# Kernel tuning notes

Hardware: AMD Instinct MI355X
Metric: run time of the kernel (lower is better)

The kernel has to match this reference:

```python
import jax, jax.numpy as jnp
import numpy as np

VOCAB = 128
N_LAYERS = 4
HEAD_DIM = 128
N_HEADS = 16
PAD = 127
HIDDEN = N_HEADS * HEAD_DIM
B, S = 1, 2048
SCALE = 1.0 / float(np.sqrt(HEAD_DIM))


def _intervals(boundary):
    # torch: interval = cumsum(boundary)+1; shifted = roll(1); shifted[:,0]=interval[:,0]
    idx = jnp.cumsum(boundary.astype(jnp.int32), axis=-1) + 1
    sh = jnp.roll(idx, 1, axis=-1)
    return sh.at[:, 0].set(idx[:, 0])


def _build_mask(tokens, segment_mask, specials_mask):
    # Combined causal & padding & word & segment mask, cache_size=0, distances=0.
    word_int = _intervals(specials_mask)            # [B,S]
    seg_bound = ~segment_mask                       # [B,S]
    seg_int = _intervals(seg_bound)                 # [B,S]
    q = jnp.arange(S)[:, None]
    kv = jnp.arange(S)[None, :]
    causal = q >= kv                                # [S,S]
    dist_neg = (q - kv) < 0                         # mask_*_distance = 0 term
    nonpad = tokens != PAD                          # [B,S]
    padm = nonpad[:, :, None] & nonpad[:, None, :]  # [B,S,S]
    wordm = specials_mask[:, None, :] | dist_neg[None] | (word_int[:, :, None] == word_int[:, None, :])
    segm = seg_bound[:, None, :] | dist_neg[None] | (seg_int[:, :, None] == seg_int[:, None, :])
    return causal[None] & padm & wordm & segm       # [B,S,S]


def _attention(h, mask):
    # q=k=v=h (no projections in DummyModel); flex_attention default scale 1/sqrt(D)
    x = h.reshape(B, S, N_HEADS, HEAD_DIM)
    scores = jnp.einsum('bqhd,bkhd->bhqk', x, x) * SCALE
    neg = jnp.finfo(scores.dtype).min
    scores = jnp.where(mask[:, None], scores, neg)
    probs = jax.nn.softmax(scores, axis=-1)
    # fully-masked rows (e.g. padding queries) -> zero output, matching flex_attention
    row_valid = jnp.any(mask, axis=-1)              # [B,S]
    probs = jnp.where(row_valid[:, None, :, None], probs, 0.0)
    out = jnp.einsum('bhqk,bkhd->bqhd', probs, x)
    return out.reshape(B, S, HIDDEN)


def setup_inputs() -> dict:
    key = jax.random.key(0)
    k1, k2, k3, k4, k5, k6 = jax.random.split(key, 6)
    tokens = jax.random.randint(k1, (B, S), 0, PAD)          # 0..126, no pad tokens
    segment_mask = jax.random.bernoulli(k2, 0.98, (B, S))
    specials_mask = jax.random.bernoulli(k3, 0.2, (B, S))    # True = word boundary/special
    emb_w = jax.random.normal(k4, (VOCAB, HIDDEN), jnp.float32) * 0.02
    lm_w = jax.random.normal(k5, (VOCAB, HIDDEN), jnp.float32) * 0.02
    lm_b = jnp.zeros((VOCAB,), jnp.float32)
    seg_w = jax.random.normal(k6, (2, HIDDEN), jnp.float32) * 0.02
    seg_b = jnp.zeros((2,), jnp.float32)
    return {"tokens": tokens, "segment_mask": segment_mask, "specials_mask": specials_mask,
            "emb_w": emb_w, "lm_w": lm_w, "lm_b": lm_b, "seg_w": seg_w, "seg_b": seg_b}


def reference(tokens, segment_mask, specials_mask, emb_w, lm_w, lm_b, seg_w, seg_b):
    mask = _build_mask(tokens, segment_mask, specials_mask)
    hidden = emb_w[tokens]                                   # [B,S,HIDDEN]
    for _ in range(N_LAYERS):
        hidden = _attention(hidden, mask)
    logits = hidden @ lm_w.T + lm_b                          # [B,S,VOCAB]
    logits_segment = hidden @ seg_w.T + seg_b                # [B,S,2]
    return logits, logits_segment
```

## Files before the change

kernel.cpp:

```cpp
#include <hip/hip_runtime.h>

#define S 2048
#define HID 2048
#define NH 16
#define DH 128
#define VOC 128
#define LCAP 128
#define K2EXP 0.12752551286084112f
#define RTHR 62.0f
#define NEGS -3.0e38f

typedef __bf16 bf16_t;
typedef __attribute__((ext_vector_type(8))) __bf16 bf16x8;
typedef __attribute__((ext_vector_type(4))) __bf16 bf16x4;
typedef __attribute__((ext_vector_type(4))) float f32x4;
typedef __attribute__((ext_vector_type(16))) float f32x16;

typedef __attribute__((address_space(1))) unsigned int guint;
typedef __attribute__((address_space(3))) unsigned int luint;

#define MFMA16 __builtin_amdgcn_mfma_f32_16x16x32_bf16
#define MFMA32 __builtin_amdgcn_mfma_f32_32x32x16_bf16

__device__ __forceinline__ void gl_lds16(const void* g, void* l) {
  __builtin_amdgcn_global_load_lds((guint*)(unsigned long long)g,
                                   (luint*)(unsigned)(unsigned long long)l,
                                   16, 0, 0);
}

__device__ __forceinline__ unsigned cvtpk(float lo, float hi) {
  unsigned r;
  asm("v_cvt_pk_bf16_f32 %0, %1, %2" : "=v"(r) : "v"(lo), "v"(hi));
  return r;
}
__device__ __forceinline__ void plswap(unsigned& a, unsigned& b) {
  asm volatile("v_permlane32_swap_b32 %0, %1" : "+v"(a), "+v"(b));
}
__device__ __forceinline__ bf16x8 mk8(unsigned d0, unsigned d1, unsigned d2, unsigned d3) {
  union { unsigned u[4]; bf16x8 v; } x;
  x.u[0] = d0; x.u[1] = d1; x.u[2] = d2; x.u[3] = d3;
  return x.v;
}


__global__ __launch_bounds__(256) void maskprep2(const int* __restrict__ tokens,
                                                 const unsigned char* __restrict__ seg,
                                                 const unsigned char* __restrict__ spc,
                                                 int4* __restrict__ mi,
                                                 int* __restrict__ lq,
                                                 unsigned long long* __restrict__ lmask,
                                                 int2* __restrict__ smeta) {
  __shared__ int ssp[257], ssg[257], smw[257], sms[257], sfl[257];
  __shared__ int fpre[2048];
  __shared__ int ns64[64];
  __shared__ unsigned long long lmk[32];
  __shared__ int cdet[2];
  int t = threadIdx.x;
  if (t < 2) cdet[t] = 0;
  if (t < 32) lmk[t] = 0ull;
  __syncthreads();
  {
    int nz = ((t & 3) != 0 && seg[t]) ? 1 : 0;
    int fc = ((t & 3) == 3 && seg[t] == 0x3f) ? 1 : 0;
    if (nz) atomicAdd(&cdet[0], 1);
    if (fc) atomicAdd(&cdet[1], 1);
  }
  __syncthreads();
  int lay = (cdet[1] > 8) ? 2 : ((cdet[0] > 4) ? 1 : 0);
  auto getb = [&](const unsigned char* p, int i) -> int {
    if (lay == 1) return p[i] != 0;
    if (lay == 2) return ((const float*)p)[i] != 0.f;
    return ((const int*)p)[i] != 0;
  };
  int base = t * 8;
  int spv[8], sgv[8], npv[8], fv[8];
  int a = 0, b = 0, mw = 0, ms = 0, fs = 0;
  for (int j = 0; j < 8; j++) {
    int i = base + j;
    spv[j] = getb(spc, i);
    sgv[j] = 1 - getb(seg, i);
    npv[j] = (tokens[i] != 127) ? 1 : 0;
    fv[j] = spv[j] & sgv[j] & npv[j];
    a += spv[j]; b += sgv[j]; fs += fv[j];
    if (i >= 1 && spv[j]) mw = (i + 1 > mw) ? i + 1 : mw;
    if (i >= 1 && sgv[j]) ms = (i + 1 > ms) ? i + 1 : ms;
  }
  ssp[t + 1] = a; ssg[t + 1] = b; smw[t + 1] = mw; sms[t + 1] = ms; sfl[t + 1] = fs;
  if (t == 0) { ssp[0] = 0; ssg[0] = 0; smw[0] = 0; sms[0] = 0; sfl[0] = 0; }
  __syncthreads();
  for (int off = 1; off < 256; off <<= 1) {
    int v0 = 0, v1 = 0, v2 = 0, v3 = 0, v4 = 0;
    if (t + 1 > off) { v0 = ssp[t+1-off]; v1 = ssg[t+1-off]; v2 = smw[t+1-off]; v3 = sms[t+1-off]; v4 = sfl[t+1-off]; }
    __syncthreads();
    ssp[t + 1] += v0; ssg[t + 1] += v1;
    if (v2 > smw[t + 1]) smw[t + 1] = v2;
    if (v3 > sms[t + 1]) sms[t + 1] = v3;
    sfl[t + 1] += v4;
    __syncthreads();
  }
  if ((t & 3) == 0) {
    int ws = smw[t], ss = sms[t];
    ns64[t >> 2] = ws < ss ? ws : ss;
  }
  int esp = ssp[t], esg = ssg[t], ef = sfl[t];
  for (int j = 0; j < 8; j++) {
    int i = base + j;
    int wint = (i == 0) ? (1 + spv[j]) : (1 + esp);
    int sint = (i == 0) ? (1 + sgv[j]) : (1 + esg);
    mi[i] = make_int4(npv[j] | (spv[j] << 1) | (sgv[j] << 2), wint, sint, 0);
    fpre[i] = ef;
    int lqv = (fv[j] && ef < LCAP) ? ef : -1;
    lq[i] = lqv;
    if (lqv >= 0) atomicOr(&lmk[i >> 6], 1ull << (i & 63));
    esp += spv[j]; esg += sgv[j]; ef += fv[j];
  }
  __syncthreads();
  if (t < 32) lmask[t] = lmk[t];
  if (t < 64) {
    int nsTile = ns64[t] >> 5;
    int lc = fpre[nsTile * 32];
    if (lc > LCAP) lc = LCAP;
    smeta[t] = make_int2(nsTile, lc);
  }
}

__global__ __launch_bounds__(256) void bitgen(const int4* __restrict__ mi,
                                              unsigned* __restrict__ cmask) {
  __shared__ int4 km[32];
  int w = blockIdx.x;
  int t = threadIdx.x;
  int q = blockIdx.y * 256 + t;
  if (t < 32) km[t] = mi[w * 32 + t];
  __syncthreads();
  int4 mq = mi[q];
  unsigned word = 0;
  #pragma unroll
  for (int j = 0; j < 32; j++) {
    int kv = w * 32 + j;
    int4 mk = km[j];
    bool v = ((mq.x & mk.x) & 1) &&
             ((mk.x & 2) || (mq.y == mk.y)) &&
             ((mk.x & 4) || (mq.z == mk.z)) &&
             (kv <= q);
    word |= (v ? 1u : 0u) << j;
  }
  cmask[(size_t)w * S + q] = word;
}

__global__ __launch_bounds__(256) void embedT2(const int* __restrict__ tokens,
                                               const float* __restrict__ emb,
                                               const int* __restrict__ lq,
                                               const unsigned long long* __restrict__ lmask,
                                               bf16_t* __restrict__ hb, bf16_t* __restrict__ vtb,
                                               bf16_t* __restrict__ hbL, bf16_t* __restrict__ vtbL) {
  __shared__ bf16_t tile[64 * 136];
  int tid = threadIdx.x;
  int q0 = blockIdx.x * 64, h = blockIdx.y;
  int ql = tid >> 2, d0 = (tid & 3) * 32;
  int tok = tokens[q0 + ql];
  const float4* src = (const float4*)(emb + (size_t)tok * HID + h * DH + d0);
  bf16x8 ob[4];
  #pragma unroll
  for (int i = 0; i < 8; i++) {
    float4 f = src[i];
    ob[i >> 1][(i & 1) * 4 + 0] = (bf16_t)f.x;
    ob[i >> 1][(i & 1) * 4 + 1] = (bf16_t)f.y;
    ob[i >> 1][(i & 1) * 4 + 2] = (bf16_t)f.z;
    ob[i >> 1][(i & 1) * 4 + 3] = (bf16_t)f.w;
  }
  #pragma unroll
  for (int i = 0; i < 4; i++)
    *(bf16x8*)(hb + (size_t)(q0 + ql) * HID + h * DH + d0 + i * 8) = ob[i];
  #pragma unroll
  for (int i = 0; i < 4; i++)
    #pragma unroll
    for (int j = 0; j < 8; j++) tile[ql * 136 + d0 + i * 8 + j] = ob[i][j];
  __syncthreads();
  {
    int tl = tid >> 7, d = tid & 127;
    bf16_t* vt = vtb + ((size_t)(h * 64) + 2 * blockIdx.x + tl) * 4096;
    #pragma unroll
    for (int c = 0; c < 4; c++) {
      bf16x8 v;
      #pragma unroll
      for (int e = 0; e < 8; e++)
        v[e] = tile[(32 * tl + 8 * (c ^ (d & 3)) + e) * 136 + d];
      *(bf16x8*)(vt + d * 32 + c * 8) = v;
    }
  }
  unsigned long long lm = lmask[q0 >> 6];
  while (lm) {
    int r = __builtin_ctzll(lm);
    lm &= lm - 1;
    int li = lq[q0 + r];
    if (li >= 0 && tid < 128) {
      bf16_t vv = tile[r * 136 + tid];
      hbL[(size_t)li * HID + h * DH + tid] = vv;
      vtbL[((size_t)(h * 4) + (li >> 5)) * 4096 + tid * 32 + (((li & 31) >> 3) ^ (tid & 3)) * 8 + (li & 7)] = vv;
    }
  }
}

__global__ __launch_bounds__(64, 2) void attn8(const bf16_t* __restrict__ hb,
                                               const bf16_t* __restrict__ vtb,
                                               const bf16_t* __restrict__ hbL,
                                               const bf16_t* __restrict__ vtbL,
                                               const unsigned* __restrict__ cmask,
                                               const int4* __restrict__ mi,
                                               const int2* __restrict__ smeta,
                                               const int* __restrict__ lq,
                                               const unsigned long long* __restrict__ lmask,
                                               bf16_t* __restrict__ ob,
                                               bf16_t* __restrict__ ovtb,
                                               bf16_t* __restrict__ obL,
                                               bf16_t* __restrict__ ovtbL,
                                               int writeT) {
  __shared__ __align__(16) char lds_raw[32768];

  int h = blockIdx.x, st = blockIdx.y;
  int2 sm = smeta[st];
  int nsT = sm.x, lcount = sm.y;
  int nNear = st + 1 - nsT;
  int nLT = (lcount + 31) >> 5;
  int nIter = nNear + nLT;

  int l = threadIdx.x, l31 = l & 31, hi = l >> 5;
  int q0 = 32 * st, q = q0 + l31;
  int npq = mi[q].x & 1;

  bf16x8 qf[8];
  {
    const bf16_t* hq = hb + (size_t)q * HID + h * DH;
    #pragma unroll
    for (int ks = 0; ks < 8; ks++) qf[ks] = *(const bf16x8*)(hq + ks * 16 + hi * 8);
  }

  f32x16 acc[4];
  #pragma unroll
  for (int i = 0; i < 4; i++)
    #pragma unroll
    for (int r = 0; r < 16; r++) acc[i][r] = 0.f;
  float m = -1e30f, lsum = 0.f;
  int swz = l31 & 7;

  auto STAGE = [&](int i, int b) {
    const bf16_t* Kbase; const bf16_t* Vtile;
    if (i < nNear) {
      int t = nsT + i;
      Kbase = hb + (size_t)(t * 32) * HID + h * DH;
      Vtile = vtb + ((size_t)(h * 64) + t) * 4096;
    } else {
      int j = i - nNear;
      Kbase = hbL + (size_t)(j * 32) * HID + h * DH;
      Vtile = vtbL + ((size_t)(h * 4) + j) * 4096;
    }
    bf16_t* Kb = (bf16_t*)(lds_raw + b * 16384);
    bf16_t* Vb = (bf16_t*)(lds_raw + b * 16384 + 8192);
    #pragma unroll
    for (int i2 = 0; i2 < 8; i2++) {
      int rowK = i2 * 4 + (l >> 4); int chK = (l & 15) ^ (rowK & 7);
      gl_lds16(Kbase + (size_t)rowK * HID + chK * 8, Kb + i2 * 512);
    }
    #pragma unroll
    for (int i2 = 0; i2 < 8; i2++)
      gl_lds16(Vtile + i2 * 512 + l * 8, Vb + i2 * 512);
  };

  auto getmask = [&](int i) -> unsigned {
    if (i < nNear) return cmask[(size_t)(nsT + i) * S + q];
    int rem = lcount - (i - nNear) * 32;
    unsigned w0 = (rem >= 32) ? 0xffffffffu : ((rem <= 0) ? 0u : ((1u << rem) - 1u));
    return npq ? w0 : 0u;
  };

  STAGE(0, 0);
  for (int i = 0; i < nIter; i++) {
    int b = i & 1;
    if (i + 1 < nIter) {
      STAGE(i + 1, b ^ 1);
      asm volatile("s_waitcnt vmcnt(16)" ::: "memory");
    } else {
      asm volatile("s_waitcnt vmcnt(0)" ::: "memory");
    }
    unsigned w0 = getmask(i);

    if (__any(w0 != 0u)) {
      const bf16_t* Kb = (const bf16_t*)(lds_raw + b * 16384);
      const bf16_t* Vb = (const bf16_t*)(lds_raw + b * 16384 + 8192);
      f32x16 s;
      #pragma unroll
      for (int r = 0; r < 16; r++) s[r] = 0.f;
      const bf16_t* kp = Kb + l31 * 128;
      #pragma unroll
      for (int ks = 0; ks < 8; ks++) {
        bf16x8 kf = *(const bf16x8*)(kp + (((2 * ks + hi) ^ swz) * 8));
        s = MFMA32(kf, qf[ks], s, 0, 0, 0);
      }

      float sv[16];
      float mx = NEGS;
      #pragma unroll
      for (int r = 0; r < 16; r++) {
        int bit = (r & 3) + 8 * (r >> 2) + 4 * hi;
        sv[r] = ((w0 >> bit) & 1u) ? s[r] : NEGS;
        mx = fmaxf(mx, sv[r]);
      }
      mx = fmaxf(mx, __shfl_xor(mx, 32, 64));
      if (__any(mx > m + RTHR)) {
        float mn = fmaxf(m, mx);
        float al = exp2f((m - mn) * K2EXP);
        m = mn; lsum *= al;
        #pragma unroll
        for (int r = 0; r < 16; r++) {
          float alr = __shfl(al, (r & 3) + 8 * (r >> 2) + 4 * hi, 64);
          #pragma unroll
          for (int d = 0; d < 4; d++) acc[d][r] *= alr;
        }
      }
      float mk = m * K2EXP;
      float p[16], ps = 0.f;
      #pragma unroll
      for (int r = 0; r < 16; r++) {
        p[r] = exp2f(__builtin_fmaf(sv[r], K2EXP, -mk));
        ps += p[r];
      }
      ps += __shfl_xor(ps, 32, 64);
      lsum += ps;

      bf16x8 pa[2];
      {
        unsigned a0 = cvtpk(p[0], p[1]),   a1 = cvtpk(p[2], p[3]);
        unsigned b0 = cvtpk(p[4], p[5]),   b1 = cvtpk(p[6], p[7]);
        unsigned a2 = cvtpk(p[8], p[9]),   a3 = cvtpk(p[10], p[11]);
        unsigned b2 = cvtpk(p[12], p[13]), b3 = cvtpk(p[14], p[15]);
        plswap(a0, b0); plswap(a1, b1); plswap(a2, b2); plswap(a3, b3);
        pa[0] = mk8(a0, a1, b0, b1);
        pa[1] = mk8(a2, a3, b2, b3);
      }

      #pragma unroll
      for (int db = 0; db < 4; db++) {
        const bf16_t* vr = Vb + (32 * db + l31) * 32;
        #pragma unroll
        for (int ks = 0; ks < 2; ks++) {
          bf16x8 vf = *(const bf16x8*)(vr + (((2 * ks + hi) ^ (l31 & 3)) * 8));
          acc[db] = MFMA32(pa[ks], vf, acc[db], 0, 0, 0);
        }
      }
    }
  }

  bf16_t* tl = (bf16_t*)lds_raw;
  float inv = (lsum > 0.f) ? 1.f / lsum : 0.f;
  #pragma unroll
  for (int r = 0; r < 16; r++) {
    int qr = (r & 3) + 8 * (r >> 2) + 4 * hi;
    float ivr = __shfl(inv, qr, 64);
    #pragma unroll
    for (int db = 0; db < 4; db++)
      tl[qr * 132 + db * 32 + l31] = (bf16_t)(acc[db][r] * ivr);
  }
  {
    int c4 = l & 3;
    #pragma unroll
    for (int g = 0; g < 2; g++) {
      int row = g * 16 + (l >> 2);
      #pragma unroll
      for (int k = 0; k < 4; k++) {
        bf16x8 v = *(const bf16x8*)(tl + row * 132 + c4 * 32 + k * 8);
        *(bf16x8*)(ob + (size_t)(q0 + row) * HID + h * DH + c4 * 32 + k * 8) = v;
      }
    }
  }
  if (writeT) {
    bf16_t* vt = ovtb + ((size_t)(h * 64) + st) * 4096;
    #pragma unroll
    for (int s = 0; s < 8; s++) {
      int d = s * 16 + (l >> 2);
      bf16x8 v;
      #pragma unroll
      for (int e = 0; e < 8; e++)
        v[e] = tl[(8 * ((l & 3) ^ (d & 3)) + e) * 132 + d];
      *(bf16x8*)(vt + s * 512 + l * 8) = v;
    }
    unsigned lm32 = (unsigned)(lmask[st >> 1] >> ((st & 1) * 32));
    while (lm32) {
      int r = __builtin_ctz(lm32);
      lm32 &= lm32 - 1;
      int li = lq[q0 + r];
      if (li >= 0) {
        #pragma unroll
        for (int half = 0; half < 2; half++) {
          int dd = l + 64 * half;
          bf16_t vv = tl[r * 132 + dd];
          obL[(size_t)li * HID + h * DH + dd] = vv;
          ovtbL[((size_t)(h * 4) + (li >> 5)) * 4096 + dd * 32 + (((li & 31) >> 3) ^ (dd & 3)) * 8 + (li & 7)] = vv;
        }
      }
    }
  }
}

__global__ __launch_bounds__(256) void wcvt(const float* __restrict__ w, bf16_t* __restrict__ wb) {
  int i = blockIdx.x * 256 + threadIdx.x;
  float4 f = ((const float4*)w)[i];
  bf16x4 v;
  v[0] = (bf16_t)f.x; v[1] = (bf16_t)f.y; v[2] = (bf16_t)f.z; v[3] = (bf16_t)f.w;
  *(bf16x4*)(wb + (size_t)i * 4) = v;
}

__global__ __launch_bounds__(256) void lmseg_head(const bf16_t* __restrict__ hb,
                                                  const bf16_t* __restrict__ wbf,
                                                  const float* __restrict__ bias,
                                                  const float* __restrict__ sw,
                                                  const float* __restrict__ sb,
                                                  float* __restrict__ out,
                                                  float* __restrict__ outseg) {
  __shared__ float red[4][16][130];
  int tid = threadIdx.x;
  int w = tid >> 6, l = tid & 63, l16 = l & 15, g = l >> 4;
  int t0 = blockIdx.x * 16;
  f32x4 acc[8];
  #pragma unroll
  for (int i = 0; i < 8; i++) acc[i] = (f32x4){0.f, 0.f, 0.f, 0.f};
  const bf16_t* arow = hb + (size_t)(t0 + l16) * HID + w * 512;
  for (int k0 = 0; k0 < 512; k0 += 32) {
    bf16x8 af = *(const bf16x8*)(arow + k0 + g * 8);
    #pragma unroll
    for (int vt = 0; vt < 8; vt++) {
      bf16x8 bf_ = *(const bf16x8*)(wbf + (size_t)(vt * 16 + l16) * HID + w * 512 + k0 + g * 8);
      acc[vt] = MFMA16(af, bf_, acc[vt], 0, 0, 0);
    }
  }
  #pragma unroll
  for (int vt = 0; vt < 8; vt++)
    #pragma unroll
    for (int r = 0; r < 4; r++)
      red[w][4 * g + r][vt * 16 + l16] = acc[vt][r];
  __syncthreads();
  int q = tid >> 4, vc = (tid & 15) * 8;
  #pragma unroll
  for (int j = 0; j < 8; j++) {
    float s = red[0][q][vc + j] + red[1][q][vc + j] + red[2][q][vc + j] + red[3][q][vc + j];
    out[(size_t)(t0 + q) * VOC + vc + j] = s + bias[vc + j];
  }
  {
    int c = tid & 15;
    const bf16_t* hrow = hb + (size_t)(t0 + q) * HID + c * 128;
    float s0 = 0.f, s1 = 0.f;
    #pragma unroll
    for (int i = 0; i < 16; i++) {
      bf16x8 v = *(const bf16x8*)(hrow + i * 8);
      const float4* w0p = (const float4*)(sw + c * 128 + i * 8);
      const float4* w1p = (const float4*)(sw + HID + c * 128 + i * 8);
      float4 x0 = w0p[0], x1 = w0p[1], y0 = w1p[0], y1 = w1p[1];
      s0 += (float)v[0]*x0.x + (float)v[1]*x0.y + (float)v[2]*x0.z + (float)v[3]*x0.w
          + (float)v[4]*x1.x + (float)v[5]*x1.y + (float)v[6]*x1.z + (float)v[7]*x1.w;
      s1 += (float)v[0]*y0.x + (float)v[1]*y0.y + (float)v[2]*y0.z + (float)v[3]*y0.w
          + (float)v[4]*y1.x + (float)v[5]*y1.y + (float)v[6]*y1.z + (float)v[7]*y1.w;
    }
    #pragma unroll
    for (int off = 1; off < 16; off <<= 1) {
      s0 += __shfl_xor(s0, off, 64);
      s1 += __shfl_xor(s1, off, 64);
    }
    if (c == 0) {
      outseg[(size_t)(t0 + q) * 2] = s0 + sb[0];
      outseg[(size_t)(t0 + q) * 2 + 1] = s1 + sb[1];
    }
  }
}

extern "C" void kernel_launch(void* const* d_in, const int* in_sizes, int n_in,
                              void* d_out, int out_size, void* d_ws, size_t ws_size,
                              hipStream_t stream) {
  const int* tokens = (const int*)d_in[0];
  const unsigned char* seg = (const unsigned char*)d_in[1];
  const unsigned char* spc = (const unsigned char*)d_in[2];
  const float* emb_w = (const float*)d_in[3];
  const float* lm_w = (const float*)d_in[4];
  const float* lm_b = (const float*)d_in[5];
  const float* seg_w = (const float*)d_in[6];
  const float* seg_b = (const float*)d_in[7];

  char* ws = (char*)d_ws;
  int4* mi = (int4*)ws;
  unsigned* cmask = (unsigned*)(ws + (1u << 20));
  int* lq = (int*)(ws + (1u << 20) + (512u << 10));
  unsigned long long* lmask = (unsigned long long*)(ws + (1u << 20) + (520u << 10));
  int2* smeta = (int2*)(ws + (1u << 20) + (524u << 10));
  bf16_t* wbf = (bf16_t*)(ws + (2u << 20));
  bf16_t* hbLA  = (bf16_t*)(ws + (3u << 20));
  bf16_t* hbLB  = (bf16_t*)(ws + (3u << 20) + (512u << 10));
  bf16_t* vtbLA = (bf16_t*)(ws + (4u << 20));
  bf16_t* vtbLB = (bf16_t*)(ws + (4u << 20) + (512u << 10));
  bf16_t* hbA  = (bf16_t*)(ws + (8u << 20));
  bf16_t* hbB  = (bf16_t*)(ws + (16u << 20));
  bf16_t* vtbA = (bf16_t*)(ws + (24u << 20));
  bf16_t* vtbB = (bf16_t*)(ws + (32u << 20));
  float* out = (float*)d_out;

  maskprep2<<<1, 256, 0, stream>>>(tokens, seg, spc, mi, lq, lmask, smeta);
  bitgen<<<dim3(64, 8), 256, 0, stream>>>(mi, cmask);
  embedT2<<<dim3(S / 64, NH), 256, 0, stream>>>(tokens, emb_w, lq, lmask, hbA, vtbA, hbLA, vtbLA);

  bf16_t* cur = hbA;   bf16_t* curV = vtbA;
  bf16_t* nxt = hbB;   bf16_t* nxtV = vtbB;
  bf16_t* curL = hbLA; bf16_t* curLV = vtbLA;
  bf16_t* nxtL = hbLB; bf16_t* nxtLV = vtbLB;
  for (int L = 0; L < 4; L++) {
    attn8<<<dim3(NH, 64), 64, 0, stream>>>(cur, curV, curL, curLV, cmask, mi, smeta, lq, lmask,
                                           nxt, nxtV, nxtL, nxtLV, (L < 3) ? 1 : 0);
    bf16_t* t1 = cur; cur = nxt; nxt = t1;
    bf16_t* t2 = curV; curV = nxtV; nxtV = t2;
    bf16_t* t3 = curL; curL = nxtL; nxtL = t3;
    bf16_t* t4 = curLV; curLV = nxtLV; nxtLV = t4;
  }

  wcvt<<<(VOC * HID / 4) / 256, 256, 0, stream>>>(lm_w, wbf);
  lmseg_head<<<S / 16, 256, 0, stream>>>(cur, wbf, lm_b, seg_w, seg_b, out, out + (size_t)S * VOC);
}
```

Measured before the change: 137.3 us.

## Fuse embedding and four attention layers into one persistent kernel with flag sync

Replaces the separate embedding kernel and four per-layer attention launches with a single kernel. Blocks signal per-layer completion through global atomic flags and wait only on the earlier query tiles of the same head, so a tile can start its next layer without a grid-wide barrier. Each block keeps its own query fragment in registers across layers, and every layer's activations go to a separate buffer so stale data is never reread. This removes launch gaps and kernel-boundary drains. In exchange it relies on all 1024 blocks being co-resident to avoid deadlock, and it adds spin-wait and fence overhead.

```diff
diff --git a/kernel.cpp b/kernel.cpp
--- a/kernel.cpp
+++ b/kernel.cpp
@@ -41,7 +41,6 @@
   x.u[0] = d0; x.u[1] = d1; x.u[2] = d2; x.u[3] = d3;
   return x.v;
 }
-
 
 __global__ __launch_bounds__(256) void maskprep2(const int* __restrict__ tokens,
                                                  const unsigned char* __restrict__ seg,
@@ -147,75 +146,21 @@
   cmask[(size_t)w * S + q] = word;
 }
 
-__global__ __launch_bounds__(256) void embedT2(const int* __restrict__ tokens,
-                                               const float* __restrict__ emb,
-                                               const int* __restrict__ lq,
-                                               const unsigned long long* __restrict__ lmask,
-                                               bf16_t* __restrict__ hb, bf16_t* __restrict__ vtb,
-                                               bf16_t* __restrict__ hbL, bf16_t* __restrict__ vtbL) {
-  __shared__ bf16_t tile[64 * 136];
-  int tid = threadIdx.x;
-  int q0 = blockIdx.x * 64, h = blockIdx.y;
-  int ql = tid >> 2, d0 = (tid & 3) * 32;
-  int tok = tokens[q0 + ql];
-  const float4* src = (const float4*)(emb + (size_t)tok * HID + h * DH + d0);
-  bf16x8 ob[4];
-  #pragma unroll
-  for (int i = 0; i < 8; i++) {
-    float4 f = src[i];
-    ob[i >> 1][(i & 1) * 4 + 0] = (bf16_t)f.x;
-    ob[i >> 1][(i & 1) * 4 + 1] = (bf16_t)f.y;
-    ob[i >> 1][(i & 1) * 4 + 2] = (bf16_t)f.z;
-    ob[i >> 1][(i & 1) * 4 + 3] = (bf16_t)f.w;
-  }
-  #pragma unroll
-  for (int i = 0; i < 4; i++)
-    *(bf16x8*)(hb + (size_t)(q0 + ql) * HID + h * DH + d0 + i * 8) = ob[i];
-  #pragma unroll
-  for (int i = 0; i < 4; i++)
-    #pragma unroll
-    for (int j = 0; j < 8; j++) tile[ql * 136 + d0 + i * 8 + j] = ob[i][j];
-  __syncthreads();
-  {
-    int tl = tid >> 7, d = tid & 127;
-    bf16_t* vt = vtb + ((size_t)(h * 64) + 2 * blockIdx.x + tl) * 4096;
-    #pragma unroll
-    for (int c = 0; c < 4; c++) {
-      bf16x8 v;
-      #pragma unroll
-      for (int e = 0; e < 8; e++)
-        v[e] = tile[(32 * tl + 8 * (c ^ (d & 3)) + e) * 136 + d];
-      *(bf16x8*)(vt + d * 32 + c * 8) = v;
-    }
-  }
-  unsigned long long lm = lmask[q0 >> 6];
-  while (lm) {
-    int r = __builtin_ctzll(lm);
-    lm &= lm - 1;
-    int li = lq[q0 + r];
-    if (li >= 0 && tid < 128) {
-      bf16_t vv = tile[r * 136 + tid];
-      hbL[(size_t)li * HID + h * DH + tid] = vv;
-      vtbL[((size_t)(h * 4) + (li >> 5)) * 4096 + tid * 32 + (((li & 31) >> 3) ^ (tid & 3)) * 8 + (li & 7)] = vv;
-    }
-  }
-}
-
-__global__ __launch_bounds__(64, 2) void attn8(const bf16_t* __restrict__ hb,
-                                               const bf16_t* __restrict__ vtb,
-                                               const bf16_t* __restrict__ hbL,
-                                               const bf16_t* __restrict__ vtbL,
-                                               const unsigned* __restrict__ cmask,
-                                               const int4* __restrict__ mi,
-                                               const int2* __restrict__ smeta,
-                                               const int* __restrict__ lq,
-                                               const unsigned long long* __restrict__ lmask,
-                                               bf16_t* __restrict__ ob,
-                                               bf16_t* __restrict__ ovtb,
-                                               bf16_t* __restrict__ obL,
-                                               bf16_t* __restrict__ ovtbL,
-                                               int writeT) {
+__global__ __launch_bounds__(64, 2) void fused_net(const int* __restrict__ tokens,
+                                                   const float* __restrict__ emb,
+                                                   const unsigned* __restrict__ cmask,
+                                                   const int4* __restrict__ mi,
+                                                   const int2* __restrict__ smeta,
+                                                   const int* __restrict__ lq,
+                                                   const unsigned long long* __restrict__ lmask,
+                                                   bf16_t* __restrict__ hbBase,
+                                                   bf16_t* __restrict__ vtbBase,
+                                                   bf16_t* __restrict__ lBase,
+                                                   unsigned* __restrict__ flg) {
   __shared__ __align__(16) char lds_raw[32768];
+
+  const size_t HBN = (size_t)S * HID;
+  const size_t LBN = (size_t)LCAP * HID;
 
   int h = blockIdx.x, st = blockIdx.y;
   int2 sm = smeta[st];
@@ -227,176 +172,236 @@
   int l = threadIdx.x, l31 = l & 31, hi = l >> 5;
   int q0 = 32 * st, q = q0 + l31;
   int npq = mi[q].x & 1;
-
+  int swz = l31 & 7;
+
+  bf16_t* tl = (bf16_t*)lds_raw;
   bf16x8 qf[8];
+
+  auto emit = [&](int s, bool wT) {
+    bf16_t* ohb = hbBase + (size_t)s * HBN;
+    int c4 = l & 3;
+    #pragma unroll
+    for (int g = 0; g < 2; g++) {
+      int row = g * 16 + (l >> 2);
+      #pragma unroll
+      for (int k = 0; k < 4; k++) {
+        bf16x8 v = *(const bf16x8*)(tl + row * 132 + c4 * 32 + k * 8);
+        *(bf16x8*)(ohb + (size_t)(q0 + row) * HID + h * DH + c4 * 32 + k * 8) = v;
+      }
+    }
+    if (wT) {
+      bf16_t* vt = vtbBase + (size_t)s * HBN + ((size_t)(h * 64) + st) * 4096;
+      #pragma unroll
+      for (int s2 = 0; s2 < 8; s2++) {
+        int d = s2 * 16 + (l >> 2);
+        bf16x8 v;
+        #pragma unroll
+        for (int e = 0; e < 8; e++)
+          v[e] = tl[(8 * ((l & 3) ^ (d & 3)) + e) * 132 + d];
+        *(bf16x8*)(vt + s2 * 512 + l * 8) = v;
+      }
+      bf16_t* ohbL = lBase + (size_t)s * (2 * LBN);
+      bf16_t* ovtL = ohbL + LBN;
+      unsigned lm32 = (unsigned)(lmask[st >> 1] >> ((st & 1) * 32));
+      while (lm32) {
+        int r = __builtin_ctz(lm32);
+        lm32 &= lm32 - 1;
+        int li = lq[q0 + r];
+        if (li >= 0) {
+          #pragma unroll
+          for (int half = 0; half < 2; half++) {
+            int dd = l + 64 * half;
+            bf16_t vv = tl[r * 132 + dd];
+            ohbL[(size_t)li * HID + h * DH + dd] = vv;
+            ovtL[((size_t)(h * 4) + (li >> 5)) * 4096 + dd * 32 + (((li & 31) >> 3) ^ (dd & 3)) * 8 + (li & 7)] = vv;
+          }
+        }
+      }
+    }
+  };
+
+  auto load_qf = [&]() {
+    #pragma unroll
+    for (int ks = 0; ks < 8; ks++)
+      qf[ks] = *(const bf16x8*)(tl + l31 * 132 + ks * 16 + hi * 8);
+    asm volatile("s_waitcnt lgkmcnt(0)" ::: "memory");
+  };
+
+  auto set_flag = [&](int s) {
+    __threadfence();
+    if (l == 0)
+      __hip_atomic_store(flg + ((size_t)s * NH + h) * 64 + st, 1u,
+                         __ATOMIC_RELEASE, __HIP_MEMORY_SCOPE_AGENT);
+  };
+
+  auto wait_stage = [&](int s) {
+    const unsigned* f = flg + ((size_t)s * NH + h) * 64;
+    int idx = (l <= st) ? l : st;
+    for (;;) {
+      unsigned v = __hip_atomic_load(f + idx, __ATOMIC_RELAXED, __HIP_MEMORY_SCOPE_AGENT);
+      if (__all(v != 0)) break;
+      __builtin_amdgcn_s_sleep(1);
+    }
+    __threadfence();
+  };
+
   {
-    const bf16_t* hq = hb + (size_t)q * HID + h * DH;
-    #pragma unroll
-    for (int ks = 0; ks < 8; ks++) qf[ks] = *(const bf16x8*)(hq + ks * 16 + hi * 8);
-  }
-
-  f32x16 acc[4];
-  #pragma unroll
-  for (int i = 0; i < 4; i++)
-    #pragma unroll
-    for (int r = 0; r < 16; r++) acc[i][r] = 0.f;
-  float m = -1e30f, lsum = 0.f;
-  int swz = l31 & 7;
-
-  auto STAGE = [&](int i, int b) {
-    const bf16_t* Kbase; const bf16_t* Vtile;
-    if (i < nNear) {
-      int t = nsT + i;
-      Kbase = hb + (size_t)(t * 32) * HID + h * DH;
-      Vtile = vtb + ((size_t)(h * 64) + t) * 4096;
-    } else {
-      int j = i - nNear;
-      Kbase = hbL + (size_t)(j * 32) * HID + h * DH;
-      Vtile = vtbL + ((size_t)(h * 4) + j) * 4096;
-    }
-    bf16_t* Kb = (bf16_t*)(lds_raw + b * 16384);
-    bf16_t* Vb = (bf16_t*)(lds_raw + b * 16384 + 8192);
-    #pragma unroll
-    for (int i2 = 0; i2 < 8; i2++) {
-      int rowK = i2 * 4 + (l >> 4); int chK = (l & 15) ^ (rowK & 7);
-      gl_lds16(Kbase + (size_t)rowK * HID + chK * 8, Kb + i2 * 512);
-    }
-    #pragma unroll
-    for (int i2 = 0; i2 < 8; i2++)
-      gl_lds16(Vtile + i2 * 512 + l * 8, Vb + i2 * 512);
-  };
-
-  auto getmask = [&](int i) -> unsigned {
-    if (i < nNear) return cmask[(size_t)(nsT + i) * S + q];
-    int rem = lcount - (i - nNear) * 32;
-    unsigned w0 = (rem >= 32) ? 0xffffffffu : ((rem <= 0) ? 0u : ((1u << rem) - 1u));
-    return npq ? w0 : 0u;
-  };
-
-  STAGE(0, 0);
-  for (int i = 0; i < nIter; i++) {
-    int b = i & 1;
-    if (i + 1 < nIter) {
-      STAGE(i + 1, b ^ 1);
-      asm volatile("s_waitcnt vmcnt(16)" ::: "memory");
-    } else {
-      asm volatile("s_waitcnt vmcnt(0)" ::: "memory");
-    }
-    unsigned w0 = getmask(i);
-
-    if (__any(w0 != 0u)) {
-      const bf16_t* Kb = (const bf16_t*)(lds_raw + b * 16384);
-      const bf16_t* Vb = (const bf16_t*)(lds_raw + b * 16384 + 8192);
-      f32x16 s;
-      #pragma unroll
-      for (int r = 0; r < 16; r++) s[r] = 0.f;
-      const bf16_t* kp = Kb + l31 * 128;
-      #pragma unroll
-      for (int ks = 0; ks < 8; ks++) {
-        bf16x8 kf = *(const bf16x8*)(kp + (((2 * ks + hi) ^ swz) * 8));
-        s = MFMA32(kf, qf[ks], s, 0, 0, 0);
-      }
-
-      float sv[16];
-      float mx = NEGS;
-      #pragma unroll
-      for (int r = 0; r < 16; r++) {
-        int bit = (r & 3) + 8 * (r >> 2) + 4 * hi;
-        sv[r] = ((w0 >> bit) & 1u) ? s[r] : NEGS;
-        mx = fmaxf(mx, sv[r]);
-      }
-      mx = fmaxf(mx, __shfl_xor(mx, 32, 64));
-      if (__any(mx > m + RTHR)) {
-        float mn = fmaxf(m, mx);
-        float al = exp2f((m - mn) * K2EXP);
-        m = mn; lsum *= al;
+    int row = l >> 1, hf = l & 1;
+    int tok = tokens[q0 + row];
+    const float4* src = (const float4*)(emb + (size_t)tok * HID + h * DH + hf * 64);
+    #pragma unroll
+    for (int k = 0; k < 8; k++) {
+      float4 f0 = src[2 * k], f1 = src[2 * k + 1];
+      #pragma unroll
+      for (int e = 0; e < 4; e++) {
+        float fe = e == 0 ? f0.x : e == 1 ? f0.y : e == 2 ? f0.z : f0.w;
+        tl[row * 132 + hf * 64 + k * 8 + e] = (bf16_t)fe;
+      }
+      #pragma unroll
+      for (int e = 0; e < 4; e++) {
+        float fe = e == 0 ? f1.x : e == 1 ? f1.y : e == 2 ? f1.z : f1.w;
+        tl[row * 132 + hf * 64 + k * 8 + 4 + e] = (bf16_t)fe;
+      }
+    }
+  }
+  emit(0, true);
+  load_qf();
+  set_flag(0);
+
+  for (int L = 0; L < 4; L++) {
+    wait_stage(L);
+    const bf16_t* ihb  = hbBase + (size_t)L * HBN;
+    const bf16_t* ivtb = vtbBase + (size_t)L * HBN;
+    const bf16_t* ihbL = lBase + (size_t)L * (2 * LBN);
+    const bf16_t* ivtL = ihbL + LBN;
+
+    auto STAGE = [&](int i, int b) {
+      const bf16_t* Kbase; const bf16_t* Vtile;
+      if (i < nNear) {
+        int t = nsT + i;
+        Kbase = ihb + (size_t)(t * 32) * HID + h * DH;
+        Vtile = ivtb + ((size_t)(h * 64) + t) * 4096;
+      } else {
+        int j = i - nNear;
+        Kbase = ihbL + (size_t)(j * 32) * HID + h * DH;
+        Vtile = ivtL + ((size_t)(h * 4) + j) * 4096;
+      }
+      bf16_t* Kb = (bf16_t*)(lds_raw + b * 16384);
+      bf16_t* Vb = (bf16_t*)(lds_raw + b * 16384 + 8192);
+      #pragma unroll
+      for (int i2 = 0; i2 < 8; i2++) {
+        int rowK = i2 * 4 + (l >> 4); int chK = (l & 15) ^ (rowK & 7);
+        gl_lds16(Kbase + (size_t)rowK * HID + chK * 8, Kb + i2 * 512);
+      }
+      #pragma unroll
+      for (int i2 = 0; i2 < 8; i2++)
+        gl_lds16(Vtile + i2 * 512 + l * 8, Vb + i2 * 512);
+    };
+
+    auto getmask = [&](int i) -> unsigned {
+      if (i < nNear) return cmask[(size_t)(nsT + i) * S + q];
+      int rem = lcount - (i - nNear) * 32;
+      unsigned w0 = (rem >= 32) ? 0xffffffffu : ((rem <= 0) ? 0u : ((1u << rem) - 1u));
+      return npq ? w0 : 0u;
+    };
+
+    f32x16 acc[4];
+    #pragma unroll
+    for (int i = 0; i < 4; i++)
+      #pragma unroll
+      for (int r = 0; r < 16; r++) acc[i][r] = 0.f;
+    float m = -1e30f, lsum = 0.f;
+
+    STAGE(0, 0);
+    for (int i = 0; i < nIter; i++) {
+      int b = i & 1;
+      if (i + 1 < nIter) {
+        STAGE(i + 1, b ^ 1);
+        asm volatile("s_waitcnt vmcnt(16)" ::: "memory");
+      } else {
+        asm volatile("s_waitcnt vmcnt(0)" ::: "memory");
+      }
+      unsigned w0 = getmask(i);
+
+      if (__any(w0 != 0u)) {
+        const bf16_t* Kb = (const bf16_t*)(lds_raw + b * 16384);
+        const bf16_t* Vb = (const bf16_t*)(lds_raw + b * 16384 + 8192);
+        f32x16 s;
+        #pragma unroll
+        for (int r = 0; r < 16; r++) s[r] = 0.f;
+        const bf16_t* kp = Kb + l31 * 128;
+        #pragma unroll
+        for (int ks = 0; ks < 8; ks++) {
+          bf16x8 kf = *(const bf16x8*)(kp + (((2 * ks + hi) ^ swz) * 8));
+          s = MFMA32(kf, qf[ks], s, 0, 0, 0);
+        }
+
+        float sv[16];
+        float mx = NEGS;
         #pragma unroll
         for (int r = 0; r < 16; r++) {
-          float alr = __shfl(al, (r & 3) + 8 * (r >> 2) + 4 * hi, 64);
+          int bit = (r & 3) + 8 * (r >> 2) + 4 * hi;
+          sv[r] = ((w0 >> bit) & 1u) ? s[r] : NEGS;
+          mx = fmaxf(mx, sv[r]);
+        }
+        mx = fmaxf(mx, __shfl_xor(mx, 32, 64));
+        if (__any(mx > m + RTHR)) {
+          float mn = fmaxf(m, mx);
+          float al = exp2f((m - mn) * K2EXP);
+          m = mn; lsum *= al;
           #pragma unroll
-          for (int d = 0; d < 4; d++) acc[d][r] *= alr;
-        }
-      }
-      float mk = m * K2EXP;
-      float p[16], ps = 0.f;
-      #pragma unroll
-      for (int r = 0; r < 16; r++) {
-        p[r] = exp2f(__builtin_fmaf(sv[r], K2EXP, -mk));
-        ps += p[r];
-      }
-      ps += __shfl_xor(ps, 32, 64);
-      lsum += ps;
-
-      bf16x8 pa[2];
-      {
-        unsigned a0 = cvtpk(p[0], p[1]),   a1 = cvtpk(p[2], p[3]);
-        unsigned b0 = cvtpk(p[4], p[5]),   b1 = cvtpk(p[6], p[7]);
-        unsigned a2 = cvtpk(p[8], p[9]),   a3 = cvtpk(p[10], p[11]);
-        unsigned b2 = cvtpk(p[12], p[13]), b3 = cvtpk(p[14], p[15]);
-        plswap(a0, b0); plswap(a1, b1); plswap(a2, b2); plswap(a3, b3);
-        pa[0] = mk8(a0, a1, b0, b1);
-        pa[1] = mk8(a2, a3, b2, b3);
-      }
-
-      #pragma unroll
-      for (int db = 0; db < 4; db++) {
-        const bf16_t* vr = Vb + (32 * db + l31) * 32;
+          for (int r = 0; r < 16; r++) {
+            float alr = __shfl(al, (r & 3) + 8 * (r >> 2) + 4 * hi, 64);
+            #pragma unroll
+            for (int d = 0; d < 4; d++) acc[d][r] *= alr;
+          }
+        }
+        float mk = m * K2EXP;
+        float p[16], ps = 0.f;
         #pragma unroll
-        for (int ks = 0; ks < 2; ks++) {
-          bf16x8 vf = *(const bf16x8*)(vr + (((2 * ks + hi) ^ (l31 & 3)) * 8));
-          acc[db] = MFMA32(pa[ks], vf, acc[db], 0, 0, 0);
-        }
-      }
-    }
-  }
-
-  bf16_t* tl = (bf16_t*)lds_raw;
-  float inv = (lsum > 0.f) ? 1.f / lsum : 0.f;
-  #pragma unroll
-  for (int r = 0; r < 16; r++) {
-    int qr = (r & 3) + 8 * (r >> 2) + 4 * hi;
-    float ivr = __shfl(inv, qr, 64);
-    #pragma unroll
-    for (int db = 0; db < 4; db++)
-      tl[qr * 132 + db * 32 + l31] = (bf16_t)(acc[db][r] * ivr);
-  }
-  {
-    int c4 = l & 3;
-    #pragma unroll
-    for (int g = 0; g < 2; g++) {
-      int row = g * 16 + (l >> 2);
-      #pragma unroll
-      for (int k = 0; k < 4; k++) {
-        bf16x8 v = *(const bf16x8*)(tl + row * 132 + c4 * 32 + k * 8);
-        *(bf16x8*)(ob + (size_t)(q0 + row) * HID + h * DH + c4 * 32 + k * 8) = v;
-      }
-    }
-  }
-  if (writeT) {
-    bf16_t* vt = ovtb + ((size_t)(h * 64) + st) * 4096;
-    #pragma unroll
-    for (int s = 0; s < 8; s++) {
-      int d = s * 16 + (l >> 2);
-      bf16x8 v;
-      #pragma unroll
-      for (int e = 0; e < 8; e++)
-        v[e] = tl[(8 * ((l & 3) ^ (d & 3)) + e) * 132 + d];
-      *(bf16x8*)(vt + s * 512 + l * 8) = v;
-    }
-    unsigned lm32 = (unsigned)(lmask[st >> 1] >> ((st & 1) * 32));
-    while (lm32) {
-      int r = __builtin_ctz(lm32);
-      lm32 &= lm32 - 1;
-      int li = lq[q0 + r];
-      if (li >= 0) {
+        for (int r = 0; r < 16; r++) {
+          p[r] = exp2f(__builtin_fmaf(sv[r], K2EXP, -mk));
+          ps += p[r];
+        }
+        ps += __shfl_xor(ps, 32, 64);
+        lsum += ps;
+
+        bf16x8 pa[2];
+        {
+          unsigned a0 = cvtpk(p[0], p[1]),   a1 = cvtpk(p[2], p[3]);
+          unsigned b0 = cvtpk(p[4], p[5]),   b1 = cvtpk(p[6], p[7]);
+          unsigned a2 = cvtpk(p[8], p[9]),   a3 = cvtpk(p[10], p[11]);
+          unsigned b2 = cvtpk(p[12], p[13]), b3 = cvtpk(p[14], p[15]);
+          plswap(a0, b0); plswap(a1, b1); plswap(a2, b2); plswap(a3, b3);
+          pa[0] = mk8(a0, a1, b0, b1);
+          pa[1] = mk8(a2, a3, b2, b3);
+        }
+
         #pragma unroll
-        for (int half = 0; half < 2; half++) {
-          int dd = l + 64 * half;
-          bf16_t vv = tl[r * 132 + dd];
-          obL[(size_t)li * HID + h * DH + dd] = vv;
-          ovtbL[((size_t)(h * 4) + (li >> 5)) * 4096 + dd * 32 + (((li & 31) >> 3) ^ (dd & 3)) * 8 + (li & 7)] = vv;
-        }
-      }
+        for (int db = 0; db < 4; db++) {
+          const bf16_t* vr = Vb + (32 * db + l31) * 32;
+          #pragma unroll
+          for (int ks = 0; ks < 2; ks++) {
+            bf16x8 vf = *(const bf16x8*)(vr + (((2 * ks + hi) ^ (l31 & 3)) * 8));
+            acc[db] = MFMA32(pa[ks], vf, acc[db], 0, 0, 0);
+          }
+        }
+      }
+    }
+
+    float inv = (lsum > 0.f) ? 1.f / lsum : 0.f;
+    #pragma unroll
+    for (int r = 0; r < 16; r++) {
+      int qr = (r & 3) + 8 * (r >> 2) + 4 * hi;
+      float ivr = __shfl(inv, qr, 64);
+      #pragma unroll
+      for (int db = 0; db < 4; db++)
+        tl[qr * 132 + db * 32 + l31] = (bf16_t)(acc[db][r] * ivr);
+    }
+    emit(L + 1, L < 3);
+    if (L < 3) {
+      load_qf();
+      set_flag(L + 1);
     }
   }
 }
@@ -490,33 +495,18 @@
   unsigned long long* lmask = (unsigned long long*)(ws + (1u << 20) + (520u << 10));
   int2* smeta = (int2*)(ws + (1u << 20) + (524u << 10));
   bf16_t* wbf = (bf16_t*)(ws + (2u << 20));
-  bf16_t* hbLA  = (bf16_t*)(ws + (3u << 20));
-  bf16_t* hbLB  = (bf16_t*)(ws + (3u << 20) + (512u << 10));
-  bf16_t* vtbLA = (bf16_t*)(ws + (4u << 20));
-  bf16_t* vtbLB = (bf16_t*)(ws + (4u << 20) + (512u << 10));
-  bf16_t* hbA  = (bf16_t*)(ws + (8u << 20));
-  bf16_t* hbB  = (bf16_t*)(ws + (16u << 20));
-  bf16_t* vtbA = (bf16_t*)(ws + (24u << 20));
-  bf16_t* vtbB = (bf16_t*)(ws + (32u << 20));
+  unsigned* flg = (unsigned*)(ws + (3u << 20));
+  bf16_t* hbBase  = (bf16_t*)(ws + (16u << 20));
+  bf16_t* vtbBase = (bf16_t*)(ws + (56u << 20));
+  bf16_t* lBase   = (bf16_t*)(ws + (88u << 20));
   float* out = (float*)d_out;
 
+  hipMemsetAsync(flg, 0, 4 * NH * 64 * sizeof(unsigned), stream);
   maskprep2<<<1, 256, 0, stream>>>(tokens, seg, spc, mi, lq, lmask, smeta);
   bitgen<<<dim3(64, 8), 256, 0, stream>>>(mi, cmask);
-  embedT2<<<dim3(S / 64, NH), 256, 0, stream>>>(tokens, emb_w, lq, lmask, hbA, vtbA, hbLA, vtbLA);
-
-  bf16_t* cur = hbA;   bf16_t* curV = vtbA;
-  bf16_t* nxt = hbB;   bf16_t* nxtV = vtbB;
-  bf16_t* curL = hbLA; bf16_t* curLV = vtbLA;
-  bf16_t* nxtL = hbLB; bf16_t* nxtLV = vtbLB;
-  for (int L = 0; L < 4; L++) {
-    attn8<<<dim3(NH, 64), 64, 0, stream>>>(cur, curV, curL, curLV, cmask, mi, smeta, lq, lmask,
-                                           nxt, nxtV, nxtL, nxtLV, (L < 3) ? 1 : 0);
-    bf16_t* t1 = cur; cur = nxt; nxt = t1;
-    bf16_t* t2 = curV; curV = nxtV; nxtV = t2;
-    bf16_t* t3 = curL; curL = nxtL; nxtL = t3;
-    bf16_t* t4 = curLV; curLV = nxtLV; nxtLV = t4;
-  }
-
   wcvt<<<(VOC * HID / 4) / 256, 256, 0, stream>>>(lm_w, wbf);
-  lmseg_head<<<S / 16, 256, 0, stream>>>(cur, wbf, lm_b, seg_w, seg_b, out, out + (size_t)S * VOC);
-}
+  fused_net<<<dim3(NH, 64), 64, 0, stream>>>(tokens, emb_w, cmask, mi, smeta, lq, lmask,
+                                             hbBase, vtbBase, lBase, flg);
+  bf16_t* hbF = hbBase + (size_t)4 * S * HID;
+  lmseg_head<<<S / 16, 256, 0, stream>>>(hbF, wbf, lm_b, seg_w, seg_b, out, out + (size_t)S * VOC);
+}
```

New measurement: 463.7 us. 238% more time.
